# Kernel optimization log

Measured on AMD Instinct MI355X. Metric: run time of the kernel, lower is better.

Reference implementation:

```python
import jax, jax.numpy as jnp
import numpy as np

BATCH, INPUT_SIZE, NUM_UNITS = 64, 256, 768
UNFOLDS = 6

def setup_inputs() -> dict:
    key = jax.random.key(0)
    ks = jax.random.split(key, 12)
    F, H = INPUT_SIZE, NUM_UNITS
    inputs = jax.random.normal(ks[0], (BATCH, F), dtype=jnp.float32)
    state = jax.random.normal(ks[1], (BATCH, H), dtype=jnp.float32)
    sensory_mu = jax.random.uniform(ks[2], (F, H), dtype=jnp.float32) * 0.5 + 0.3
    sensory_sigma = jax.random.uniform(ks[3], (F, H), dtype=jnp.float32) * 5.0 + 3.0
    sensory_W = jax.random.uniform(ks[4], (F, H), dtype=jnp.float32, minval=0.01, maxval=1.0)
    sensory_erev = (2.0 * jax.random.randint(ks[5], (F, H), 0, 2) - 1.0).astype(jnp.float32)
    mu = jax.random.uniform(ks[6], (H, H), dtype=jnp.float32) * 0.5 + 0.3
    sigma = jax.random.uniform(ks[7], (H, H), dtype=jnp.float32) * 5.0 + 3.0
    W = jax.random.uniform(ks[8], (H, H), dtype=jnp.float32, minval=0.01, maxval=1.0)
    erev = (2.0 * jax.random.randint(ks[9], (H, H), 0, 2) - 1.0).astype(jnp.float32)
    vleak = jax.random.uniform(ks[10], (H,), dtype=jnp.float32) * 0.4 - 0.2
    gleak = jnp.ones((H,), dtype=jnp.float32)          # gleak_init_min == gleak_init_max == 1
    cm_t = jnp.full((H,), 0.5, dtype=jnp.float32)      # cm_init_min == cm_init_max == 0.5
    input_w = jnp.ones((F,), dtype=jnp.float32)        # Affine mapping weight (ones)
    input_b = jnp.zeros((F,), dtype=jnp.float32)       # Affine mapping bias (zeros)
    return dict(inputs=inputs, state=state, input_w=input_w, input_b=input_b,
                sensory_mu=sensory_mu, sensory_sigma=sensory_sigma,
                sensory_W=sensory_W, sensory_erev=sensory_erev,
                mu=mu, sigma=sigma, W=W, erev=erev,
                vleak=vleak, gleak=gleak, cm_t=cm_t)

def reference(inputs, state, input_w, input_b, sensory_mu, sensory_sigma,
              sensory_W, sensory_erev, mu, sigma, W, erev, vleak, gleak, cm_t):
    x = inputs * input_w + input_b                                   # (B, F)
    # sensory pathway: (B, F, H) broadcast sigmoid, reduced over F
    s_act = sensory_W * jax.nn.sigmoid(sensory_sigma * (x[:, :, None] - sensory_mu))
    w_num_sensory = jnp.sum(s_act * sensory_erev, axis=1)            # (B, H)
    w_den_sensory = jnp.sum(s_act, axis=1)                           # (B, H)

    def step(v_pre, _):
        act = W * jax.nn.sigmoid(sigma * (v_pre[:, :, None] - mu))   # (B, H_pre, H_post)
        w_num = jnp.sum(act * erev, axis=1) + w_num_sensory          # (B, H)
        w_den = jnp.sum(act, axis=1) + w_den_sensory                 # (B, H)
        numerator = cm_t * v_pre + gleak * vleak + w_num
        denominator = cm_t + gleak + w_den
        return numerator / denominator, None

    v_pre, _ = jax.lax.scan(step, state, None, length=UNFOLDS)
    return (v_pre, v_pre)  # (outputs, next_state)
```

## Files before the change

### kernel.cpp

```cpp
#include <hip/hip_runtime.h>


constexpr int B_ = 64;
constexpr int F_ = 256;
constexpr int H_ = 768;
constexpr int UNFOLDS_ = 6;

constexpr int NS  = 8;
constexpr int ISL = H_ / NS;
constexpr int FSL = F_ / NS;
constexpr int JG  = 96;
constexpr int STEP_BLOCKS = JG * NS;
constexpr int SENS_BLOCKS = JG * NS;
constexpr int FIN_BLOCKS  = (B_ * H_) / 256;
constexpr int TILE_STEP = (H_ / 32) * (H_ / 32);
constexpr int TILE_SENS = (F_ / 32) * (H_ / 32);

__global__ __launch_bounds__(256) void prep_k(
    const float* __restrict__ sigma, const float* __restrict__ mu,
    const float* __restrict__ W, const float* __restrict__ erev,
    const float* __restrict__ ssig, const float* __restrict__ smu,
    const float* __restrict__ sW, const float* __restrict__ serev,
    const float* __restrict__ inputs, const float* __restrict__ iw,
    const float* __restrict__ ib,
    float4* __restrict__ pk_step,
    float4* __restrict__ pk_sens,
    float* __restrict__ xT)
{
    const int tid = threadIdx.x;
    const float L2E = 1.44269504088896f;
    int blk = blockIdx.x;

    if (blk < TILE_STEP + TILE_SENS) {
        const bool sens = blk >= TILE_STEP;
        if (sens) blk -= TILE_STEP;
        const int ti = blk / 24, tj = blk % 24;
        const int i0 = ti * 32, j0 = tj * 32;
        const float* A0 = sens ? ssig : sigma;
        const float* A1 = sens ? smu : mu;
        const float* A2 = sens ? sW : W;
        const float* A3 = sens ? serev : erev;
        float4* out = sens ? pk_sens : pk_step;
        const int ILEN = sens ? F_ : H_;

        __shared__ float tsg[32][33], tmu[32][33], tw[32][33], te[32][33];
        const int col = tid & 31;
#pragma unroll
        for (int k = 0; k < 4; ++k) {
            int row = (tid >> 5) + k * 8;
            int idx = (i0 + row) * H_ + j0 + col;
            tsg[row][col] = A0[idx];
            tmu[row][col] = A1[idx];
            tw [row][col] = A2[idx];
            te [row][col] = A3[idx];
        }
        __syncthreads();
#pragma unroll
        for (int k = 0; k < 4; ++k) {
            int jj = (tid >> 5) + k * 8;
            int ii = tid & 31;
            float sg2 = tsg[ii][jj] * L2E;
            float m   = tmu[ii][jj];
            float w   = tw[ii][jj];
            float e   = te[ii][jj];
            float4 v;
            v.x = sg2 * m;
            v.y = -sg2;
            v.z = w;
            v.w = w * e;
            out[(j0 + jj) * ILEN + (i0 + ii)] = v;
        }
    } else {
        for (int e = tid; e < B_ * F_; e += 256) {
            int f = e & (F_ - 1), b = e >> 8;
            xT[f * B_ + b] = fmaf(inputs[b * F_ + f], iw[f], ib[f]);
        }
    }
}

__global__ __launch_bounds__(256) void part_k(
    const float* __restrict__ v_src,
    int first,
    const float4* __restrict__ pk_step,
    const float4* __restrict__ pk_sens,
    const float* __restrict__ xT,
    float* __restrict__ step_part,
    float* __restrict__ sens_part)
{
    const int tid  = threadIdx.x;
    const int lane = tid & 63;
    const int wv   = __builtin_amdgcn_readfirstlane(tid >> 6);
    __shared__ float vs[ISL * B_];

    int sb = blockIdx.x;
    if (sb < STEP_BLOCKS) {
        const int jg = sb % JG, sl = sb / JG;
        const int i0 = sl * ISL;
        if (first) {
            for (int e = tid; e < ISL * B_; e += 256) {
                int ii = e >> 6, b = e & 63;
                vs[ii * B_ + b] = v_src[b * H_ + i0 + ii];
            }
        } else {
            for (int e = tid; e < ISL * B_; e += 256) {
                int ii = e >> 6, b = e & 63;
                vs[ii * B_ + b] = v_src[(i0 + ii) * B_ + b];
            }
        }
        __syncthreads();

        const int j = jg * 8 + wv * 2;
        const float4* p0 = pk_step + j * H_ + i0;
        const float4* p1 = p0 + H_;
        float n0 = 0.f, d0 = 0.f, n1 = 0.f, d1 = 0.f;
#pragma unroll 4
        for (int ii = 0; ii < ISL; ++ii) {
            float v  = vs[ii * B_ + lane];
            float4 a = p0[ii];
            float4 b4 = p1[ii];
            float t0 = fmaf(a.y, v, a.x);
            float t1 = fmaf(b4.y, v, b4.x);
            float s0 = __builtin_amdgcn_rcpf(1.0f + __builtin_amdgcn_exp2f(t0));
            float s1 = __builtin_amdgcn_rcpf(1.0f + __builtin_amdgcn_exp2f(t1));
            d0 = fmaf(a.z,  s0, d0);
            n0 = fmaf(a.w,  s0, n0);
            d1 = fmaf(b4.z, s1, d1);
            n1 = fmaf(b4.w, s1, n1);
        }
        float* pn = step_part + ((sl * 2 + 0) * H_) * B_;
        float* pd = step_part + ((sl * 2 + 1) * H_) * B_;
        pn[j * B_ + lane]       = n0;
        pd[j * B_ + lane]       = d0;
        pn[(j + 1) * B_ + lane] = n1;
        pd[(j + 1) * B_ + lane] = d1;
    } else {
        const int s = sb - STEP_BLOCKS;
        const int jg = s % JG, sl = s / JG;
        const int f0 = sl * FSL;
        for (int e = tid; e < FSL * B_; e += 256) {
            int ff = e >> 6, b = e & 63;
            vs[ff * B_ + b] = xT[(f0 + ff) * B_ + b];
        }
        __syncthreads();

        const int j = jg * 8 + wv * 2;
        const float4* p0 = pk_sens + j * F_ + f0;
        const float4* p1 = p0 + F_;
        float n0 = 0.f, d0 = 0.f, n1 = 0.f, d1 = 0.f;
#pragma unroll 4
        for (int ff = 0; ff < FSL; ++ff) {
            float v  = vs[ff * B_ + lane];
            float4 a = p0[ff];
            float4 b4 = p1[ff];
            float t0 = fmaf(a.y, v, a.x);
            float t1 = fmaf(b4.y, v, b4.x);
            float s0 = __builtin_amdgcn_rcpf(1.0f + __builtin_amdgcn_exp2f(t0));
            float s1 = __builtin_amdgcn_rcpf(1.0f + __builtin_amdgcn_exp2f(t1));
            d0 = fmaf(a.z,  s0, d0);
            n0 = fmaf(a.w,  s0, n0);
            d1 = fmaf(b4.z, s1, d1);
            n1 = fmaf(b4.w, s1, n1);
        }
        float* pn = sens_part + ((sl * 2 + 0) * H_) * B_;
        float* pd = sens_part + ((sl * 2 + 1) * H_) * B_;
        pn[j * B_ + lane]       = n0;
        pd[j * B_ + lane]       = d0;
        pn[(j + 1) * B_ + lane] = n1;
        pd[(j + 1) * B_ + lane] = d1;
    }
}

__global__ __launch_bounds__(256) void fin_k(
    const float* __restrict__ v_prev,
    int first,
    const float* __restrict__ step_part,
    const float* __restrict__ sens_part,
    const float* __restrict__ vleak, const float* __restrict__ gleak,
    const float* __restrict__ cm,
    float* __restrict__ vT_out,
    float* __restrict__ out0, float* __restrict__ out1, int last)
{
    const int e = blockIdx.x * 256 + threadIdx.x;
    const int b = e & 63, h = e >> 6;

    float n = 0.f, d = 0.f;
#pragma unroll
    for (int sl = 0; sl < NS; ++sl) {
        n += step_part[((sl * 2 + 0) * H_ + h) * B_ + b];
        d += step_part[((sl * 2 + 1) * H_ + h) * B_ + b];
        n += sens_part[((sl * 2 + 0) * H_ + h) * B_ + b];
        d += sens_part[((sl * 2 + 1) * H_ + h) * B_ + b];
    }
    float vp = first ? v_prev[b * H_ + h] : v_prev[h * B_ + b];
    float g  = gleak[h];
    float numer = fmaf(cm[h], vp, fmaf(g, vleak[h], n));
    float denom = cm[h] + g + d;
    float vn = numer / denom;
    vT_out[h * B_ + b] = vn;
    if (last) { out0[b * H_ + h] = vn; out1[b * H_ + h] = vn; }
}

extern "C" void kernel_launch(void* const* d_in, const int* in_sizes, int n_in,
                              void* d_out, int out_size, void* d_ws, size_t ws_size,
                              hipStream_t stream) {
    const float* inputs = (const float*)d_in[0];
    const float* state  = (const float*)d_in[1];
    const float* iw     = (const float*)d_in[2];
    const float* ib     = (const float*)d_in[3];
    const float* smu    = (const float*)d_in[4];
    const float* ssig   = (const float*)d_in[5];
    const float* sW     = (const float*)d_in[6];
    const float* serev  = (const float*)d_in[7];
    const float* mu     = (const float*)d_in[8];
    const float* sigma  = (const float*)d_in[9];
    const float* W      = (const float*)d_in[10];
    const float* erev   = (const float*)d_in[11];
    const float* vleak  = (const float*)d_in[12];
    const float* gleak  = (const float*)d_in[13];
    const float* cm     = (const float*)d_in[14];
    float* out = (float*)d_out;

    float* ws = (float*)d_ws;
    float4* pk_step = (float4*)ws;
    float4* pk_sens = pk_step + H_ * H_;
    float*  xT      = (float*)(pk_sens + H_ * F_);
    float*  step_part = xT + F_ * B_;
    float*  sens_part = step_part + NS * 2 * H_ * B_;
    float*  vT0       = sens_part + NS * 2 * H_ * B_;
    float*  vT1       = vT0 + H_ * B_;

    prep_k<<<TILE_STEP + TILE_SENS + 1, 256, 0, stream>>>(
        sigma, mu, W, erev, ssig, smu, sW, serev, inputs, iw, ib,
        pk_step, pk_sens, xT);

    for (int t = 0; t < UNFOLDS_; ++t) {
        const int first = (t == 0);
        const int last  = (t == UNFOLDS_ - 1);
        const float* vsrc = first ? state : ((t & 1) ? vT0 : vT1);
        float* vdst = (t & 1) ? vT1 : vT0;
        int nblk = first ? (STEP_BLOCKS + SENS_BLOCKS) : STEP_BLOCKS;
        part_k<<<nblk, 256, 0, stream>>>(vsrc, first, pk_step, pk_sens, xT,
                                         step_part, sens_part);
        fin_k<<<FIN_BLOCKS, 256, 0, stream>>>(vsrc, first, step_part, sens_part,
                                              vleak, gleak, cm, vdst,
                                              out, out + B_ * H_, last);
    }
}
```

Baseline: 213.1 us.

## Split step reduction into more slices, drop LDS staging, pre-transpose initial state

Doubles the number of input slices for the recurrent step (16 slices of 48), which doubles the number of blocks per launch. Each lane now reads its v value straight from global or cache instead of staging the slice in shared memory behind a barrier. The initial state transpose moves into the prep kernel, so part_k and fin_k no longer branch on a first-step layout. The cost is twice as many partial sums written and then read back in fin_k on every step.

Measured after the change: 315.9 us. 1.48x slower.

```diff
diff --git a/kernel.cpp b/kernel.cpp
--- a/kernel.cpp
+++ b/kernel.cpp
@@ -6,15 +6,15 @@
 constexpr int H_ = 768;
 constexpr int UNFOLDS_ = 6;
 
-constexpr int NS  = 8;
-constexpr int ISL = H_ / NS;
-constexpr int FSL = F_ / NS;
-constexpr int JG  = 96;
-constexpr int STEP_BLOCKS = JG * NS;
-constexpr int SENS_BLOCKS = JG * NS;
+constexpr int NS_STEP = 16, LI_STEP = 48;
+constexpr int NS_SENS = 8,  LF_SENS = 32;
+constexpr int JG = H_ / 8;
+constexpr int STEP_BLOCKS = JG * NS_STEP;
+constexpr int SENS_BLOCKS = JG * NS_SENS;
 constexpr int FIN_BLOCKS  = (B_ * H_) / 256;
 constexpr int TILE_STEP = (H_ / 32) * (H_ / 32);
 constexpr int TILE_SENS = (F_ / 32) * (H_ / 32);
+constexpr int PREP_BLOCKS = TILE_STEP + TILE_SENS + 1 + 3;
 
 __global__ __launch_bounds__(256) void prep_k(
     const float* __restrict__ sigma, const float* __restrict__ mu,
@@ -22,10 +22,11 @@
     const float* __restrict__ ssig, const float* __restrict__ smu,
     const float* __restrict__ sW, const float* __restrict__ serev,
     const float* __restrict__ inputs, const float* __restrict__ iw,
-    const float* __restrict__ ib,
+    const float* __restrict__ ib, const float* __restrict__ state,
     float4* __restrict__ pk_step,
     float4* __restrict__ pk_sens,
-    float* __restrict__ xT)
+    float* __restrict__ xT,
+    float* __restrict__ vT_init)
 {
     const int tid = threadIdx.x;
     const float L2E = 1.44269504088896f;
@@ -40,7 +41,7 @@
         const float* A1 = sens ? smu : mu;
         const float* A2 = sens ? sW : W;
         const float* A3 = sens ? serev : erev;
-        float4* out = sens ? pk_sens : pk_step;
+        float4* outp = sens ? pk_sens : pk_step;
         const int ILEN = sens ? F_ : H_;
 
         __shared__ float tsg[32][33], tmu[32][33], tw[32][33], te[32][33];
@@ -60,27 +61,30 @@
             int jj = (tid >> 5) + k * 8;
             int ii = tid & 31;
             float sg2 = tsg[ii][jj] * L2E;
-            float m   = tmu[ii][jj];
-            float w   = tw[ii][jj];
-            float e   = te[ii][jj];
             float4 v;
-            v.x = sg2 * m;
+            v.x = sg2 * tmu[ii][jj];
             v.y = -sg2;
-            v.z = w;
-            v.w = w * e;
-            out[(j0 + jj) * ILEN + (i0 + ii)] = v;
-        }
-    } else {
+            v.z = tw[ii][jj];
+            v.w = tw[ii][jj] * te[ii][jj];
+            outp[(j0 + jj) * ILEN + (i0 + ii)] = v;
+        }
+    } else if (blk == TILE_STEP + TILE_SENS) {
         for (int e = tid; e < B_ * F_; e += 256) {
             int f = e & (F_ - 1), b = e >> 8;
             xT[f * B_ + b] = fmaf(inputs[b * F_ + f], iw[f], ib[f]);
         }
+    } else {
+        const int vb = blk - (TILE_STEP + TILE_SENS + 1);
+        for (int e = tid; e < (B_ * H_) / 3; e += 256) {
+            int g = vb * ((B_ * H_) / 3) + e;
+            int b = g / H_, h = g % H_;
+            vT_init[h * B_ + b] = state[g];
+        }
     }
 }
 
 __global__ __launch_bounds__(256) void part_k(
-    const float* __restrict__ v_src,
-    int first,
+    const float* __restrict__ vT,
     const float4* __restrict__ pk_step,
     const float4* __restrict__ pk_sens,
     const float* __restrict__ xT,
@@ -89,46 +93,34 @@
 {
     const int tid  = threadIdx.x;
     const int lane = tid & 63;
-    const int wv   = __builtin_amdgcn_readfirstlane(tid >> 6);
-    __shared__ float vs[ISL * B_];
-
+    const int wv   = tid >> 6;
     int sb = blockIdx.x;
+
     if (sb < STEP_BLOCKS) {
         const int jg = sb % JG, sl = sb / JG;
-        const int i0 = sl * ISL;
-        if (first) {
-            for (int e = tid; e < ISL * B_; e += 256) {
-                int ii = e >> 6, b = e & 63;
-                vs[ii * B_ + b] = v_src[b * H_ + i0 + ii];
-            }
-        } else {
-            for (int e = tid; e < ISL * B_; e += 256) {
-                int ii = e >> 6, b = e & 63;
-                vs[ii * B_ + b] = v_src[(i0 + ii) * B_ + b];
-            }
-        }
-        __syncthreads();
-
+        const int i0 = sl * LI_STEP;
         const int j = jg * 8 + wv * 2;
         const float4* p0 = pk_step + j * H_ + i0;
         const float4* p1 = p0 + H_;
+        const float* vp = vT + i0 * B_ + lane;
+
         float n0 = 0.f, d0 = 0.f, n1 = 0.f, d1 = 0.f;
-#pragma unroll 4
-        for (int ii = 0; ii < ISL; ++ii) {
-            float v  = vs[ii * B_ + lane];
+#pragma unroll 8
+        for (int ii = 0; ii < LI_STEP; ++ii) {
+            float v  = vp[ii * B_];
             float4 a = p0[ii];
-            float4 b4 = p1[ii];
+            float4 c = p1[ii];
             float t0 = fmaf(a.y, v, a.x);
-            float t1 = fmaf(b4.y, v, b4.x);
+            float t1 = fmaf(c.y, v, c.x);
             float s0 = __builtin_amdgcn_rcpf(1.0f + __builtin_amdgcn_exp2f(t0));
             float s1 = __builtin_amdgcn_rcpf(1.0f + __builtin_amdgcn_exp2f(t1));
-            d0 = fmaf(a.z,  s0, d0);
-            n0 = fmaf(a.w,  s0, n0);
-            d1 = fmaf(b4.z, s1, d1);
-            n1 = fmaf(b4.w, s1, n1);
-        }
-        float* pn = step_part + ((sl * 2 + 0) * H_) * B_;
-        float* pd = step_part + ((sl * 2 + 1) * H_) * B_;
+            d0 = fmaf(a.z, s0, d0);
+            n0 = fmaf(a.w, s0, n0);
+            d1 = fmaf(c.z, s1, d1);
+            n1 = fmaf(c.w, s1, n1);
+        }
+        float* pn = step_part + (sl * 2 + 0) * H_ * B_;
+        float* pd = step_part + (sl * 2 + 1) * H_ * B_;
         pn[j * B_ + lane]       = n0;
         pd[j * B_ + lane]       = d0;
         pn[(j + 1) * B_ + lane] = n1;
@@ -136,33 +128,29 @@
     } else {
         const int s = sb - STEP_BLOCKS;
         const int jg = s % JG, sl = s / JG;
-        const int f0 = sl * FSL;
-        for (int e = tid; e < FSL * B_; e += 256) {
-            int ff = e >> 6, b = e & 63;
-            vs[ff * B_ + b] = xT[(f0 + ff) * B_ + b];
-        }
-        __syncthreads();
-
+        const int f0 = sl * LF_SENS;
         const int j = jg * 8 + wv * 2;
         const float4* p0 = pk_sens + j * F_ + f0;
         const float4* p1 = p0 + F_;
+        const float* xp = xT + f0 * B_ + lane;
+
         float n0 = 0.f, d0 = 0.f, n1 = 0.f, d1 = 0.f;
-#pragma unroll 4
-        for (int ff = 0; ff < FSL; ++ff) {
-            float v  = vs[ff * B_ + lane];
+#pragma unroll 8
+        for (int ff = 0; ff < LF_SENS; ++ff) {
+            float v  = xp[ff * B_];
             float4 a = p0[ff];
-            float4 b4 = p1[ff];
+            float4 c = p1[ff];
             float t0 = fmaf(a.y, v, a.x);
-            float t1 = fmaf(b4.y, v, b4.x);
+            float t1 = fmaf(c.y, v, c.x);
             float s0 = __builtin_amdgcn_rcpf(1.0f + __builtin_amdgcn_exp2f(t0));
             float s1 = __builtin_amdgcn_rcpf(1.0f + __builtin_amdgcn_exp2f(t1));
-            d0 = fmaf(a.z,  s0, d0);
-            n0 = fmaf(a.w,  s0, n0);
-            d1 = fmaf(b4.z, s1, d1);
-            n1 = fmaf(b4.w, s1, n1);
-        }
-        float* pn = sens_part + ((sl * 2 + 0) * H_) * B_;
-        float* pd = sens_part + ((sl * 2 + 1) * H_) * B_;
+            d0 = fmaf(a.z, s0, d0);
+            n0 = fmaf(a.w, s0, n0);
+            d1 = fmaf(c.z, s1, d1);
+            n1 = fmaf(c.w, s1, n1);
+        }
+        float* pn = sens_part + (sl * 2 + 0) * H_ * B_;
+        float* pd = sens_part + (sl * 2 + 1) * H_ * B_;
         pn[j * B_ + lane]       = n0;
         pd[j * B_ + lane]       = d0;
         pn[(j + 1) * B_ + lane] = n1;
@@ -172,7 +160,6 @@
 
 __global__ __launch_bounds__(256) void fin_k(
     const float* __restrict__ v_prev,
-    int first,
     const float* __restrict__ step_part,
     const float* __restrict__ sens_part,
     const float* __restrict__ vleak, const float* __restrict__ gleak,
@@ -182,21 +169,26 @@
 {
     const int e = blockIdx.x * 256 + threadIdx.x;
     const int b = e & 63, h = e >> 6;
+    const int o = h * B_ + b;
 
     float n = 0.f, d = 0.f;
 #pragma unroll
-    for (int sl = 0; sl < NS; ++sl) {
+    for (int sl = 0; sl < NS_STEP; ++sl) {
         n += step_part[((sl * 2 + 0) * H_ + h) * B_ + b];
         d += step_part[((sl * 2 + 1) * H_ + h) * B_ + b];
+    }
+#pragma unroll
+    for (int sl = 0; sl < NS_SENS; ++sl) {
         n += sens_part[((sl * 2 + 0) * H_ + h) * B_ + b];
         d += sens_part[((sl * 2 + 1) * H_ + h) * B_ + b];
     }
-    float vp = first ? v_prev[b * H_ + h] : v_prev[h * B_ + b];
+
+    float vp = v_prev[o];
     float g  = gleak[h];
     float numer = fmaf(cm[h], vp, fmaf(g, vleak[h], n));
     float denom = cm[h] + g + d;
     float vn = numer / denom;
-    vT_out[h * B_ + b] = vn;
+    vT_out[o] = vn;
     if (last) { out0[b * H_ + h] = vn; out1[b * H_ + h] = vn; }
 }
 
@@ -225,24 +217,25 @@
     float4* pk_sens = pk_step + H_ * H_;
     float*  xT      = (float*)(pk_sens + H_ * F_);
     float*  step_part = xT + F_ * B_;
-    float*  sens_part = step_part + NS * 2 * H_ * B_;
-    float*  vT0       = sens_part + NS * 2 * H_ * B_;
-    float*  vT1       = vT0 + H_ * B_;
-
-    prep_k<<<TILE_STEP + TILE_SENS + 1, 256, 0, stream>>>(
-        sigma, mu, W, erev, ssig, smu, sW, serev, inputs, iw, ib,
-        pk_step, pk_sens, xT);
-
+    float*  sens_part = step_part + NS_STEP * 2 * H_ * B_;
+    float*  vinit     = sens_part + NS_SENS * 2 * H_ * B_;
+    float*  vb0       = vinit + H_ * B_;
+    float*  vb1       = vb0 + H_ * B_;
+
+    prep_k<<<PREP_BLOCKS, 256, 0, stream>>>(
+        sigma, mu, W, erev, ssig, smu, sW, serev, inputs, iw, ib, state,
+        pk_step, pk_sens, xT, vinit);
+
+    const float* vsrc = vinit;
     for (int t = 0; t < UNFOLDS_; ++t) {
-        const int first = (t == 0);
-        const int last  = (t == UNFOLDS_ - 1);
-        const float* vsrc = first ? state : ((t & 1) ? vT0 : vT1);
-        float* vdst = (t & 1) ? vT1 : vT0;
-        int nblk = first ? (STEP_BLOCKS + SENS_BLOCKS) : STEP_BLOCKS;
-        part_k<<<nblk, 256, 0, stream>>>(vsrc, first, pk_step, pk_sens, xT,
+        const int last = (t == UNFOLDS_ - 1);
+        float* vdst = (t & 1) ? vb1 : vb0;
+        int nblk = (t == 0) ? (STEP_BLOCKS + SENS_BLOCKS) : STEP_BLOCKS;
+        part_k<<<nblk, 256, 0, stream>>>(vsrc, pk_step, pk_sens, xT,
                                          step_part, sens_part);
-        fin_k<<<FIN_BLOCKS, 256, 0, stream>>>(vsrc, first, step_part, sens_part,
+        fin_k<<<FIN_BLOCKS, 256, 0, stream>>>(vsrc, step_part, sens_part,
                                               vleak, gleak, cm, vdst,
                                               out, out + B_ * H_, last);
-    }
-}
+        vsrc = vdst;
+    }
+}
```
